# Optimization experiments

Hardware: AMD Instinct MI355X
Metric: run time of the kernel (lower is better)

## Reference

```python
import jax, jax.numpy as jnp
import numpy as np
import math

E_IN, E_OUT = 512, 96
B, QL, PL = 64, 128, 196

def _lin(k, shape):
    fan_in = shape[1]
    bound = 1.0 / math.sqrt(fan_in)
    k1, k2 = jax.random.split(k)
    W = jax.random.uniform(k1, shape, jnp.float32, -bound, bound)
    b = jax.random.uniform(k2, (shape[0],), jnp.float32, -bound, bound)
    return W, b

def setup_inputs() -> dict:
    key = jax.random.key(0)
    ks = jax.random.split(key, 16)
    inp = {
        'z_d_cls': jax.random.normal(ks[0], (B, E_IN), jnp.float32),
        'Z_d_tok': jax.random.normal(ks[1], (B, QL, E_IN), jnp.float32),
        'z_t_cls': jax.random.normal(ks[2], (B, E_IN), jnp.float32),
        'Z_t_tok': jax.random.normal(ks[3], (B, QL, E_IN), jnp.float32),
        'z_v_cls': jax.random.normal(ks[4], (B, E_IN), jnp.float32),
        'Z_v_patch': jax.random.normal(ks[5], (B, PL, E_IN), jnp.float32),
    }
    names = ['t_cls', 'd_cls', 'v_cls', 't_tok', 'v_patch', 'tgl_q', 'tgl_k', 'tgl_v']
    for i, n in enumerate(names):
        W, b = _lin(ks[6 + i], (E_OUT, E_IN))
        inp[f'W_{n}'] = W
        inp[f'b_{n}'] = b
    inp['ln_g'] = jnp.ones((E_OUT,), jnp.float32)
    inp['ln_b'] = jnp.zeros((E_OUT,), jnp.float32)
    return inp

def _l2n(x, eps=1e-6):
    return x / jnp.maximum(jnp.linalg.norm(x, axis=-1, keepdims=True), eps)

def _proj(x, W, b):
    return x @ W.T + b

def _layer_norm(x, g, b, eps=1e-5):
    mu = jnp.mean(x, axis=-1, keepdims=True)
    var = jnp.mean((x - mu) ** 2, axis=-1, keepdims=True)
    return (x - mu) / jnp.sqrt(var + eps) * g + b

def reference(z_d_cls, Z_d_tok, z_t_cls, Z_t_tok, z_v_cls, Z_v_patch,
              W_t_cls, b_t_cls, W_d_cls, b_d_cls, W_v_cls, b_v_cls,
              W_t_tok, b_t_tok, W_v_patch, b_v_patch,
              W_tgl_q, b_tgl_q, W_tgl_k, b_tgl_k, W_tgl_v, b_tgl_v,
              ln_g, ln_b):
    # --- TGG: global-global text/doc cosine sim [B, B]
    t = _l2n(_proj(z_t_cls, W_t_cls, b_t_cls))
    d = _l2n(_proj(z_d_cls, W_d_cls, b_d_cls))
    S_TGG = t @ d.T
    # --- TGL: cross-attention over all batch pairs
    Q = _proj(Z_d_tok, W_tgl_q, b_tgl_q)   # [b, q, h]
    K = _proj(Z_t_tok, W_tgl_k, b_tgl_k)   # [c, k, h]
    V = _proj(Z_t_tok, W_tgl_v, b_tgl_v)   # [c, k, h]
    scores = jnp.einsum('bqh,ckh->bcqk', Q, K) / math.sqrt(E_OUT)
    attn = jax.nn.softmax(scores, axis=-1)
    context = jnp.einsum('bcqk,ckh->bcqh', attn, V).mean(axis=2)  # [b, c, h]
    context = _layer_norm(context, ln_g, ln_b)
    S_TGL = jnp.einsum('ih,ijh->ij', d, _l2n(context))
    S_TIB = 0.5 * (S_TGG + S_TGL)
    # --- CGG: global-global text/vision cosine sim
    v = _l2n(_proj(z_v_cls, W_v_cls, b_v_cls))
    S_CGG = t @ v.T
    # --- CLL: token-patch max similarity
    t_tok = _l2n(_proj(Z_t_tok, W_t_tok, b_t_tok))        # [b, t, h]
    v_pat = _l2n(_proj(Z_v_patch, W_v_patch, b_v_patch))  # [c, p, h]
    sim = jnp.einsum('bth,cph->bctp', t_tok, v_pat)
    S_CLL = sim.max(axis=(-1, -2))
    S_CAB = 0.5 * (S_CGG + S_CLL)
    return S_TIB + S_CAB
```

## Files before the change

### kernel.cpp

```cpp
#include <hip/hip_runtime.h>
#include <hip/hip_bf16.h>
#include <math.h>

typedef __bf16 bf16;
typedef __attribute__((ext_vector_type(8))) __bf16 bf16x8;
typedef __attribute__((ext_vector_type(2))) float f32x2;
typedef __attribute__((ext_vector_type(4))) float f32x4;
typedef __attribute__((ext_vector_type(4))) unsigned int uint4v;

#define MFMA16(a, b, c) __builtin_amdgcn_mfma_f32_16x16x32_bf16(a, b, c, 0, 0, 0)

#define QSCALE 0.14724450f

__device__ __forceinline__ bf16x8 cvt8v(f32x4 lo, f32x4 hi) {
    bf16x8 r;
    r[0] = (bf16)lo[0]; r[1] = (bf16)lo[1]; r[2] = (bf16)lo[2]; r[3] = (bf16)lo[3];
    r[4] = (bf16)hi[0]; r[5] = (bf16)hi[1]; r[6] = (bf16)hi[2]; r[7] = (bf16)hi[3];
    return r;
}


struct ProjParams {
    const float* src[8];
    const float* W[8];
    const float* B[8];
    void* dst[8];
};

__global__ __launch_bounds__(256) void proj_kernel(ProjParams p) {
    int w = threadIdx.x >> 6, lane = threadIdx.x & 63;
    int gw = blockIdx.x * 4 + w;
    int m = lane & 15, quad = lane >> 4;

    int job, t0;
    if      (gw < 256)  { job = 3; t0 = gw; }
    else if (gw < 512)  { job = 4; t0 = gw - 256; }
    else if (gw < 768)  { job = 5; t0 = gw - 512; }
    else if (gw < 1024) { job = 6; t0 = gw - 768; }
    else if (gw < 1416) { job = 7; t0 = gw - 1024; }
    else if (gw < 1422) { int r = gw - 1416; job = r >> 1; t0 = r & 1; }
    else return;
    int r0 = t0 << 5;

    const float* X  = p.src[job] + (size_t)(r0 + m) * 512 + quad * 8;
    const float* Wf = p.W[job] + (size_t)m * 512 + quad * 8;

    f32x4 acc[2][6] = {};
    #pragma unroll
    for (int kk = 0; kk < 512; kk += 32) {
        bf16x8 a0 = cvt8v(*(const f32x4*)(X + kk),
                          *(const f32x4*)(X + kk + 4));
        bf16x8 a1 = cvt8v(*(const f32x4*)(X + 16 * 512 + kk),
                          *(const f32x4*)(X + 16 * 512 + kk + 4));
        #pragma unroll
        for (int nt = 0; nt < 6; nt++) {
            const float* wp = Wf + (size_t)nt * 16 * 512 + kk;
            bf16x8 b = cvt8v(*(const f32x4*)wp, *(const f32x4*)(wp + 4));
            acc[0][nt] = MFMA16(a0, b, acc[0][nt]);
            acc[1][nt] = MFMA16(a1, b, acc[1][nt]);
        }
    }

    bool  norm  = (job < 3) || (job >= 6);
    float scale = (job == 3) ? QSCALE : 1.0f;
    const float* Bv = p.B[job];
    float bb[6];
    #pragma unroll
    for (int nt = 0; nt < 6; nt++) bb[nt] = Bv[nt * 16 + m];

    #pragma unroll
    for (int rt = 0; rt < 2; rt++)
        #pragma unroll
        for (int nt = 0; nt < 6; nt++)
            #pragma unroll
            for (int r = 0; r < 4; r++)
                acc[rt][nt][r] = (acc[rt][nt][r] + bb[nt]) * scale;

    if (norm) {
        #pragma unroll
        for (int rt = 0; rt < 2; rt++)
            #pragma unroll
            for (int r = 0; r < 4; r++) {
                float s = 0.0f;
                #pragma unroll
                for (int nt = 0; nt < 6; nt++) s += acc[rt][nt][r] * acc[rt][nt][r];
                s += __shfl_xor(s, 1); s += __shfl_xor(s, 2);
                s += __shfl_xor(s, 4); s += __shfl_xor(s, 8);
                float inv = 1.0f / fmaxf(sqrtf(s), 1e-6f);
                #pragma unroll
                for (int nt = 0; nt < 6; nt++) acc[rt][nt][r] *= inv;
            }
    }

    if (job < 3) {
        float* dst = (float*)p.dst[job];
        #pragma unroll
        for (int rt = 0; rt < 2; rt++)
            #pragma unroll
            for (int r = 0; r < 4; r++)
                #pragma unroll
                for (int nt = 0; nt < 6; nt++)
                    dst[(size_t)(r0 + rt * 16 + quad * 4 + r) * 96 + nt * 16 + m] = acc[rt][nt][r];
    } else {
        bf16* dst = (bf16*)p.dst[job];
        #pragma unroll
        for (int rt = 0; rt < 2; rt++)
            #pragma unroll
            for (int r = 0; r < 4; r++)
                #pragma unroll
                for (int nt = 0; nt < 6; nt++)
                    dst[(size_t)(r0 + rt * 16 + quad * 4 + r) * 96 + nt * 16 + m] = (bf16)acc[rt][nt][r];
    }
}


__global__ __launch_bounds__(256) void attn_kernel(
    const bf16* __restrict__ Qg, const bf16* __restrict__ Kg, const bf16* __restrict__ Vg,
    float* __restrict__ Ctx)
{
    int pr = blockIdx.x;
    int b = pr >> 6, c = pr & 63;
    int tid = threadIdx.x, lane = tid & 63, w = tid >> 6;
    int m = lane & 15, quad = lane >> 4;
    const bf16* Q = Qg + (size_t)b * (128 * 96);
    const bf16* K = Kg + (size_t)c * (128 * 96);
    const bf16* V = Vg + (size_t)c * (128 * 96);

    __shared__ __align__(16) bf16 Klds[128 * 96];
    char* kb = (char*)Klds;
    #pragma unroll
    for (int it = 0; it < 6; it++) {
        int ch = it * 256 + tid;
        int row = ch / 12, seg = ch - row * 12;
        int addr = (row * 192 + seg * 16) ^ ((row & 7) << 4);
        *(uint4v*)(kb + addr) = *(const uint4v*)(K + ch * 8);
    }
    __syncthreads();

    int kx = (m & 7) << 4;
    f32x4 acc[2][8] = {};
    #pragma unroll
    for (int kk = 0; kk < 96; kk += 32) {
        bf16x8 a0 = *(const bf16x8*)(Q + (size_t)(w * 32 + m) * 96 + kk + quad * 8);
        bf16x8 a1 = *(const bf16x8*)(Q + (size_t)(w * 32 + 16 + m) * 96 + kk + quad * 8);
        #pragma unroll
        for (int nt = 0; nt < 8; nt++) {
            int addr = ((nt * 16 + m) * 192 + kk * 2 + quad * 16) ^ kx;
            bf16x8 bb = *(const bf16x8*)(kb + addr);
            acc[0][nt] = MFMA16(a0, bb, acc[0][nt]);
            acc[1][nt] = MFMA16(a1, bb, acc[1][nt]);
        }
    }

    unsigned vr[32];
    if (lane < 48) {
        #pragma unroll
        for (int r = 0; r < 32; r++)
            vr[r] = *(const unsigned*)(V + (size_t)(w * 32 + r) * 96 + lane * 2);
    }

    float wpart[8];
    #pragma unroll
    for (int nt = 0; nt < 8; nt++) wpart[nt] = 0.0f;
    #pragma unroll
    for (int mt = 0; mt < 2; mt++) {
        #pragma unroll
        for (int r = 0; r < 4; r++) {
            float tv[8]; float s = 0.0f;
            #pragma unroll
            for (int nt = 0; nt < 8; nt++) { tv[nt] = exp2f(acc[mt][nt][r]); s += tv[nt]; }
            s += __shfl_xor(s, 1); s += __shfl_xor(s, 2);
            s += __shfl_xor(s, 4); s += __shfl_xor(s, 8);
            float inv = __builtin_amdgcn_rcpf(s);
            #pragma unroll
            for (int nt = 0; nt < 8; nt++) wpart[nt] += tv[nt] * inv;
        }
    }
    #pragma unroll
    for (int nt = 0; nt < 8; nt++) {
        wpart[nt] += __shfl_xor(wpart[nt], 16);
        wpart[nt] += __shfl_xor(wpart[nt], 32);
    }
    __shared__ float wsum4[4][128];
    __shared__ float wk[128];
    __shared__ float ctxp[4][96];
    if (lane < 16) {
        #pragma unroll
        for (int nt = 0; nt < 8; nt++) wsum4[w][nt * 16 + lane] = wpart[nt];
    }
    __syncthreads();
    if (tid < 128) wk[tid] = wsum4[0][tid] + wsum4[1][tid] + wsum4[2][tid] + wsum4[3][tid];
    __syncthreads();
    {
        float c0 = 0.0f, c1 = 0.0f;
        if (lane < 48) {
            #pragma unroll
            for (int r = 0; r < 32; r++) {
                unsigned u = vr[r];
                float wkk = wk[w * 32 + r];
                c0 += wkk * __uint_as_float(u << 16);
                c1 += wkk * __uint_as_float(u & 0xffff0000u);
            }
            ctxp[w][lane * 2]     = c0;
            ctxp[w][lane * 2 + 1] = c1;
        }
    }
    __syncthreads();
    if (tid < 96)
        Ctx[(size_t)pr * 96 + tid] =
            (ctxp[0][tid] + ctxp[1][tid] + ctxp[2][tid] + ctxp[3][tid]) * (1.0f / 128.0f);
}


__global__ __launch_bounds__(256) void cll_kernel(
    const bf16* __restrict__ Tt, const bf16* __restrict__ Vp,
    const float* __restrict__ Ctx, const float* __restrict__ t,
    const float* __restrict__ d, const float* __restrict__ v,
    const float* __restrict__ ln_g, const float* __restrict__ ln_b,
    float* __restrict__ out)
{
    int c = blockIdx.x >> 3, bg = blockIdx.x & 7;
    int tid = threadIdx.x, lane = tid & 63, w = tid >> 6;
    int m = lane & 15, quad = lane >> 4;
    const bf16* P = Vp + (size_t)c * (196 * 96);

    __shared__ __align__(16) bf16 Plds[196 * 96];
    __shared__ float red[8][4];
    char* pb = (char*)Plds;
    for (int ch = tid; ch < 2352; ch += 256) {
        int row = ch / 12, seg = ch - row * 12;
        int addr = (row * 192 + seg * 16) ^ ((row & 7) << 4);
        *(uint4v*)(pb + addr) = *(const uint4v*)(P + ch * 8);
    }
    int rofs[13], rx[13];
    #pragma unroll
    for (int nt = 0; nt < 13; nt++) {
        int r = nt * 16 + m; if (r > 195) r = 195;
        rofs[nt] = r * 192 + quad * 16;
        rx[nt]   = (r & 7) << 4;
    }
    __syncthreads();

    for (int bi = 0; bi < 8; bi++) {
        const bf16* T = Tt + (size_t)(bg * 8 + bi) * (128 * 96);
        f32x4 acc[2][13] = {};
        #pragma unroll
        for (int kk = 0; kk < 96; kk += 32) {
            bf16x8 a0 = *(const bf16x8*)(T + (size_t)(w * 32 + m) * 96 + kk + quad * 8);
            bf16x8 a1 = *(const bf16x8*)(T + (size_t)(w * 32 + 16 + m) * 96 + kk + quad * 8);
            #pragma unroll
            for (int nt = 0; nt < 13; nt++) {
                bf16x8 bb = *(const bf16x8*)(pb + ((rofs[nt] + kk * 2) ^ rx[nt]));
                acc[0][nt] = MFMA16(a0, bb, acc[0][nt]);
                acc[1][nt] = MFMA16(a1, bb, acc[1][nt]);
            }
        }
        float mx = -3.4e38f;
        #pragma unroll
        for (int mt = 0; mt < 2; mt++)
            #pragma unroll
            for (int nt = 0; nt < 13; nt++)
                #pragma unroll
                for (int r = 0; r < 4; r++) mx = fmaxf(mx, acc[mt][nt][r]);
        #pragma unroll
        for (int dd = 1; dd < 64; dd <<= 1) mx = fmaxf(mx, __shfl_xor(mx, dd));
        if (lane == 0) red[bi][w] = mx;
    }
    __syncthreads();

    #pragma unroll
    for (int half = 0; half < 2; half++) {
        int bi = w + half * 4;
        int i  = bg * 8 + bi;
        int pr = i * 64 + c;
        float scll = fmaxf(fmaxf(red[bi][0], red[bi][1]), fmaxf(red[bi][2], red[bi][3]));
        bool act = lane < 48;
        float c0 = 0, c1 = 0, t0 = 0, t1 = 0;
        float dj0 = 0, dj1 = 0, di0 = 0, di1 = 0, v0 = 0, v1 = 0, g0 = 0, g1 = 0, bb0 = 0, bb1 = 0;
        if (act) {
            f32x2 cc  = *(const f32x2*)(Ctx + (size_t)pr * 96 + lane * 2);
            f32x2 tt  = *(const f32x2*)(t + i * 96 + lane * 2);
            f32x2 ddj = *(const f32x2*)(d + c * 96 + lane * 2);
            f32x2 ddi = *(const f32x2*)(d + i * 96 + lane * 2);
            f32x2 vv  = *(const f32x2*)(v + c * 96 + lane * 2);
            f32x2 gg  = *(const f32x2*)(ln_g + lane * 2);
            f32x2 bbv = *(const f32x2*)(ln_b + lane * 2);
            c0 = cc[0]; c1 = cc[1]; t0 = tt[0]; t1 = tt[1];
            dj0 = ddj[0]; dj1 = ddj[1]; di0 = ddi[0]; di1 = ddi[1];
            v0 = vv[0]; v1 = vv[1];
            g0 = gg[0]; g1 = gg[1]; bb0 = bbv[0]; bb1 = bbv[1];
        }
        float s = c0 + c1;
        #pragma unroll
        for (int k = 1; k < 64; k <<= 1) s += __shfl_xor(s, k);
        float mean = s * (1.0f / 96.0f);
        float e0 = act ? (c0 - mean) : 0.0f;
        float e1 = act ? (c1 - mean) : 0.0f;
        float q = e0 * e0 + e1 * e1;
        #pragma unroll
        for (int k = 1; k < 64; k <<= 1) q += __shfl_xor(q, k);
        float rstd = rsqrtf(q * (1.0f / 96.0f) + 1e-5f);
        float y0 = act ? (e0 * rstd * g0 + bb0) : 0.0f;
        float y1 = act ? (e1 * rstd * g1 + bb1) : 0.0f;
        float dot = y0 * di0 + y1 * di1;
        float ssq = y0 * y0 + y1 * y1;
        float tg  = t0 * dj0 + t1 * dj1;
        float cg  = t0 * v0 + t1 * v1;
        #pragma unroll
        for (int k = 1; k < 64; k <<= 1) {
            dot += __shfl_xor(dot, k); ssq += __shfl_xor(ssq, k);
            tg  += __shfl_xor(tg, k);  cg  += __shfl_xor(cg, k);
        }
        if (lane == 0) {
            float stgl = dot / fmaxf(sqrtf(ssq), 1e-6f);
            out[pr] = 0.5f * (tg + stgl) + 0.5f * (cg + scll);
        }
    }
}


extern "C" void kernel_launch(void* const* d_in, const int* in_sizes, int n_in,
                              void* d_out, int out_size, void* d_ws, size_t ws_size,
                              hipStream_t stream)
{
    (void)in_sizes; (void)n_in; (void)out_size; (void)ws_size;
    char* ws = (char*)d_ws;
    float* t     = (float*)(ws + 0);
    float* d     = (float*)(ws + 24576);
    float* v     = (float*)(ws + 49152);
    bf16* Qb = (bf16*)(ws + 892928);
    bf16* Kb = (bf16*)(ws + 892928 + 1572864);
    bf16* Vb = (bf16*)(ws + 892928 + 2 * 1572864);
    bf16* Tt = (bf16*)(ws + 892928 + 3 * 1572864);
    bf16* Vp = (bf16*)(ws + 892928 + 4 * 1572864);
    float* Ctx = (float*)(ws + 892928 + 4 * 1572864 + 2408448);

    ProjParams pp;
    pp.src[0] = (const float*)d_in[2];  pp.W[0] = (const float*)d_in[6];  pp.B[0] = (const float*)d_in[7];  pp.dst[0] = t;
    pp.src[1] = (const float*)d_in[0];  pp.W[1] = (const float*)d_in[8];  pp.B[1] = (const float*)d_in[9];  pp.dst[1] = d;
    pp.src[2] = (const float*)d_in[4];  pp.W[2] = (const float*)d_in[10]; pp.B[2] = (const float*)d_in[11]; pp.dst[2] = v;
    pp.src[3] = (const float*)d_in[1];  pp.W[3] = (const float*)d_in[16]; pp.B[3] = (const float*)d_in[17]; pp.dst[3] = Qb;
    pp.src[4] = (const float*)d_in[3];  pp.W[4] = (const float*)d_in[18]; pp.B[4] = (const float*)d_in[19]; pp.dst[4] = Kb;
    pp.src[5] = (const float*)d_in[3];  pp.W[5] = (const float*)d_in[20]; pp.B[5] = (const float*)d_in[21]; pp.dst[5] = Vb;
    pp.src[6] = (const float*)d_in[3];  pp.W[6] = (const float*)d_in[12]; pp.B[6] = (const float*)d_in[13]; pp.dst[6] = Tt;
    pp.src[7] = (const float*)d_in[5];  pp.W[7] = (const float*)d_in[14]; pp.B[7] = (const float*)d_in[15]; pp.dst[7] = Vp;
    hipLaunchKernelGGL(proj_kernel, dim3(356), dim3(256), 0, stream, pp);

    hipLaunchKernelGGL(attn_kernel, dim3(4096), dim3(256), 0, stream,
                       (const bf16*)Qb, (const bf16*)Kb, (const bf16*)Vb, Ctx);
    hipLaunchKernelGGL(cll_kernel, dim3(512), dim3(256), 0, stream,
                       (const bf16*)Tt, (const bf16*)Vp,
                       (const float*)Ctx, (const float*)t, (const float*)d, (const float*)v,
                       (const float*)d_in[22], (const float*)d_in[23], (float*)d_out);
}
```

Measured before the change: 264.5 us.

## Fuse projection, attention and CLL stages into one persistent kernel with grid barriers

Replaces the three kernel launches with one 256-block persistent kernel that separates its stages with atomic grid-wide barriers. It first converts the weights to bf16 once so the projection tiles read bf16 weights, then loops blocks over the projection, attention and CLL tiles. In attention each block keeps its K/V slice resident and reuses it over 16 query batches, using a padded LDS layout in place of the XOR swizzle. This removes launch gaps and repeated K/V loads, at the cost of a fixed 256-block grid that may underfill 256 CUs with 2 blocks per CU allowed, extra memset and barrier overhead, and deadlock risk if not all blocks are co-resident.

```diff
diff --git a/kernel.cpp b/kernel.cpp
--- a/kernel.cpp
+++ b/kernel.cpp
@@ -19,301 +19,314 @@
     return r;
 }
 
-
-struct ProjParams {
+__device__ __forceinline__ void grid_barrier(unsigned* bar, int slot, unsigned nblk, int tid) {
+    __syncthreads();
+    if (tid == 0) {
+        __threadfence();
+        __hip_atomic_fetch_add(&bar[slot], 1u, __ATOMIC_ACQ_REL, __HIP_MEMORY_SCOPE_AGENT);
+        while (__hip_atomic_load(&bar[slot], __ATOMIC_ACQUIRE, __HIP_MEMORY_SCOPE_AGENT) < nblk)
+            __builtin_amdgcn_s_sleep(2);
+        __threadfence();
+    }
+    __syncthreads();
+}
+
+struct MegaParams {
+    const float* W[8];
     const float* src[8];
-    const float* W[8];
     const float* B[8];
     void* dst[8];
+    bf16* Wb;
+    const bf16 *Qb, *Kb, *Vb, *Tt, *Vp;
+    float* Ctx;
+    const float *t, *d, *v, *ln_g, *ln_b;
+    float* out;
+    unsigned* bar;
 };
 
-__global__ __launch_bounds__(256) void proj_kernel(ProjParams p) {
-    int w = threadIdx.x >> 6, lane = threadIdx.x & 63;
-    int gw = blockIdx.x * 4 + w;
+
+__global__ __launch_bounds__(256, 2) void mega_kernel(MegaParams P) {
+    int tid = threadIdx.x, bid = blockIdx.x;
+    int w = tid >> 6, lane = tid & 63;
     int m = lane & 15, quad = lane >> 4;
-
-    int job, t0;
-    if      (gw < 256)  { job = 3; t0 = gw; }
-    else if (gw < 512)  { job = 4; t0 = gw - 256; }
-    else if (gw < 768)  { job = 5; t0 = gw - 512; }
-    else if (gw < 1024) { job = 6; t0 = gw - 768; }
-    else if (gw < 1416) { job = 7; t0 = gw - 1024; }
-    else if (gw < 1422) { int r = gw - 1416; job = r >> 1; t0 = r & 1; }
-    else return;
-    int r0 = t0 << 5;
-
-    const float* X  = p.src[job] + (size_t)(r0 + m) * 512 + quad * 8;
-    const float* Wf = p.W[job] + (size_t)m * 512 + quad * 8;
-
-    f32x4 acc[2][6] = {};
-    #pragma unroll
-    for (int kk = 0; kk < 512; kk += 32) {
-        bf16x8 a0 = cvt8v(*(const f32x4*)(X + kk),
-                          *(const f32x4*)(X + kk + 4));
-        bf16x8 a1 = cvt8v(*(const f32x4*)(X + 16 * 512 + kk),
-                          *(const f32x4*)(X + 16 * 512 + kk + 4));
-        #pragma unroll
-        for (int nt = 0; nt < 6; nt++) {
-            const float* wp = Wf + (size_t)nt * 16 * 512 + kk;
-            bf16x8 b = cvt8v(*(const f32x4*)wp, *(const f32x4*)(wp + 4));
-            acc[0][nt] = MFMA16(a0, b, acc[0][nt]);
-            acc[1][nt] = MFMA16(a1, b, acc[1][nt]);
-        }
-    }
-
-    bool  norm  = (job < 3) || (job >= 6);
-    float scale = (job == 3) ? QSCALE : 1.0f;
-    const float* Bv = p.B[job];
-    float bb[6];
-    #pragma unroll
-    for (int nt = 0; nt < 6; nt++) bb[nt] = Bv[nt * 16 + m];
-
-    #pragma unroll
-    for (int rt = 0; rt < 2; rt++)
-        #pragma unroll
-        for (int nt = 0; nt < 6; nt++)
-            #pragma unroll
-            for (int r = 0; r < 4; r++)
-                acc[rt][nt][r] = (acc[rt][nt][r] + bb[nt]) * scale;
-
-    if (norm) {
+    unsigned nblk = gridDim.x;
+
+    __shared__ __align__(16) char smem[37888];
+    bf16*  Klds  = (bf16*)smem;
+    float* wsum4 = (float*)(smem + 26624);
+    float* wk    = (float*)(smem + 28672);
+    float* ctxp  = (float*)(smem + 29184);
+    char*  pb    = smem;
+    float* red   = (float*)(smem + 37632);
+
+    {
+        int base = bid * 384;
+        for (int k = tid; k < 384; k += 256) {
+            int e4  = base + k;
+            int j   = e4 / 12288;
+            int off = (e4 - j * 12288) * 4;
+            f32x4 val = *(const f32x4*)(P.W[j] + off);
+            bf16* dst = P.Wb + j * 49152 + off;
+            dst[0] = (bf16)val[0]; dst[1] = (bf16)val[1];
+            dst[2] = (bf16)val[2]; dst[3] = (bf16)val[3];
+        }
+    }
+    grid_barrier(P.bar, 0, nblk, tid);
+
+    for (int tile = bid * 4 + w; tile < 1422; tile += 1024) {
+        int job, t0;
+        if      (tile < 256)  { job = 3; t0 = tile; }
+        else if (tile < 512)  { job = 4; t0 = tile - 256; }
+        else if (tile < 768)  { job = 5; t0 = tile - 512; }
+        else if (tile < 1024) { job = 6; t0 = tile - 768; }
+        else if (tile < 1416) { job = 7; t0 = tile - 1024; }
+        else                  { int r = tile - 1416; job = r >> 1; t0 = r & 1; }
+        int r0 = t0 << 5;
+        const float* X = P.src[job] + (size_t)(r0 + m) * 512 + quad * 8;
+        const bf16*  W = P.Wb + job * 49152 + (size_t)m * 512 + quad * 8;
+
+        f32x4 acc[2][6] = {};
+        #pragma unroll
+        for (int kk = 0; kk < 512; kk += 32) {
+            bf16x8 a0 = cvt8v(*(const f32x4*)(X + kk),
+                              *(const f32x4*)(X + kk + 4));
+            bf16x8 a1 = cvt8v(*(const f32x4*)(X + 16 * 512 + kk),
+                              *(const f32x4*)(X + 16 * 512 + kk + 4));
+            #pragma unroll
+            for (int nt = 0; nt < 6; nt++) {
+                bf16x8 b = *(const bf16x8*)(W + (size_t)nt * 16 * 512 + kk);
+                acc[0][nt] = MFMA16(a0, b, acc[0][nt]);
+                acc[1][nt] = MFMA16(a1, b, acc[1][nt]);
+            }
+        }
+        bool  norm  = (job < 3) || (job >= 6);
+        float scale = (job == 3) ? QSCALE : 1.0f;
+        const float* Bv = P.B[job];
+        float bb[6];
+        #pragma unroll
+        for (int nt = 0; nt < 6; nt++) bb[nt] = Bv[nt * 16 + m];
         #pragma unroll
         for (int rt = 0; rt < 2; rt++)
             #pragma unroll
-            for (int r = 0; r < 4; r++) {
-                float s = 0.0f;
-                #pragma unroll
-                for (int nt = 0; nt < 6; nt++) s += acc[rt][nt][r] * acc[rt][nt][r];
-                s += __shfl_xor(s, 1); s += __shfl_xor(s, 2);
-                s += __shfl_xor(s, 4); s += __shfl_xor(s, 8);
-                float inv = 1.0f / fmaxf(sqrtf(s), 1e-6f);
-                #pragma unroll
-                for (int nt = 0; nt < 6; nt++) acc[rt][nt][r] *= inv;
-            }
-    }
-
-    if (job < 3) {
-        float* dst = (float*)p.dst[job];
-        #pragma unroll
-        for (int rt = 0; rt < 2; rt++)
-            #pragma unroll
-            for (int r = 0; r < 4; r++)
-                #pragma unroll
-                for (int nt = 0; nt < 6; nt++)
-                    dst[(size_t)(r0 + rt * 16 + quad * 4 + r) * 96 + nt * 16 + m] = acc[rt][nt][r];
-    } else {
-        bf16* dst = (bf16*)p.dst[job];
-        #pragma unroll
-        for (int rt = 0; rt < 2; rt++)
-            #pragma unroll
-            for (int r = 0; r < 4; r++)
-                #pragma unroll
-                for (int nt = 0; nt < 6; nt++)
-                    dst[(size_t)(r0 + rt * 16 + quad * 4 + r) * 96 + nt * 16 + m] = (bf16)acc[rt][nt][r];
-    }
-}
-
-
-__global__ __launch_bounds__(256) void attn_kernel(
-    const bf16* __restrict__ Qg, const bf16* __restrict__ Kg, const bf16* __restrict__ Vg,
-    float* __restrict__ Ctx)
-{
-    int pr = blockIdx.x;
-    int b = pr >> 6, c = pr & 63;
-    int tid = threadIdx.x, lane = tid & 63, w = tid >> 6;
-    int m = lane & 15, quad = lane >> 4;
-    const bf16* Q = Qg + (size_t)b * (128 * 96);
-    const bf16* K = Kg + (size_t)c * (128 * 96);
-    const bf16* V = Vg + (size_t)c * (128 * 96);
-
-    __shared__ __align__(16) bf16 Klds[128 * 96];
-    char* kb = (char*)Klds;
-    #pragma unroll
-    for (int it = 0; it < 6; it++) {
-        int ch = it * 256 + tid;
-        int row = ch / 12, seg = ch - row * 12;
-        int addr = (row * 192 + seg * 16) ^ ((row & 7) << 4);
-        *(uint4v*)(kb + addr) = *(const uint4v*)(K + ch * 8);
-    }
-    __syncthreads();
-
-    int kx = (m & 7) << 4;
-    f32x4 acc[2][8] = {};
-    #pragma unroll
-    for (int kk = 0; kk < 96; kk += 32) {
-        bf16x8 a0 = *(const bf16x8*)(Q + (size_t)(w * 32 + m) * 96 + kk + quad * 8);
-        bf16x8 a1 = *(const bf16x8*)(Q + (size_t)(w * 32 + 16 + m) * 96 + kk + quad * 8);
-        #pragma unroll
-        for (int nt = 0; nt < 8; nt++) {
-            int addr = ((nt * 16 + m) * 192 + kk * 2 + quad * 16) ^ kx;
-            bf16x8 bb = *(const bf16x8*)(kb + addr);
-            acc[0][nt] = MFMA16(a0, bb, acc[0][nt]);
-            acc[1][nt] = MFMA16(a1, bb, acc[1][nt]);
-        }
-    }
-
-    unsigned vr[32];
-    if (lane < 48) {
-        #pragma unroll
-        for (int r = 0; r < 32; r++)
-            vr[r] = *(const unsigned*)(V + (size_t)(w * 32 + r) * 96 + lane * 2);
-    }
-
-    float wpart[8];
-    #pragma unroll
-    for (int nt = 0; nt < 8; nt++) wpart[nt] = 0.0f;
-    #pragma unroll
-    for (int mt = 0; mt < 2; mt++) {
-        #pragma unroll
-        for (int r = 0; r < 4; r++) {
-            float tv[8]; float s = 0.0f;
-            #pragma unroll
-            for (int nt = 0; nt < 8; nt++) { tv[nt] = exp2f(acc[mt][nt][r]); s += tv[nt]; }
-            s += __shfl_xor(s, 1); s += __shfl_xor(s, 2);
-            s += __shfl_xor(s, 4); s += __shfl_xor(s, 8);
-            float inv = __builtin_amdgcn_rcpf(s);
-            #pragma unroll
-            for (int nt = 0; nt < 8; nt++) wpart[nt] += tv[nt] * inv;
-        }
-    }
-    #pragma unroll
-    for (int nt = 0; nt < 8; nt++) {
-        wpart[nt] += __shfl_xor(wpart[nt], 16);
-        wpart[nt] += __shfl_xor(wpart[nt], 32);
-    }
-    __shared__ float wsum4[4][128];
-    __shared__ float wk[128];
-    __shared__ float ctxp[4][96];
-    if (lane < 16) {
-        #pragma unroll
-        for (int nt = 0; nt < 8; nt++) wsum4[w][nt * 16 + lane] = wpart[nt];
-    }
-    __syncthreads();
-    if (tid < 128) wk[tid] = wsum4[0][tid] + wsum4[1][tid] + wsum4[2][tid] + wsum4[3][tid];
-    __syncthreads();
+            for (int nt = 0; nt < 6; nt++)
+                #pragma unroll
+                for (int r = 0; r < 4; r++)
+                    acc[rt][nt][r] = (acc[rt][nt][r] + bb[nt]) * scale;
+        if (norm) {
+            #pragma unroll
+            for (int rt = 0; rt < 2; rt++)
+                #pragma unroll
+                for (int r = 0; r < 4; r++) {
+                    float s = 0.0f;
+                    #pragma unroll
+                    for (int nt = 0; nt < 6; nt++) s += acc[rt][nt][r] * acc[rt][nt][r];
+                    s += __shfl_xor(s, 1); s += __shfl_xor(s, 2);
+                    s += __shfl_xor(s, 4); s += __shfl_xor(s, 8);
+                    float inv = 1.0f / fmaxf(sqrtf(s), 1e-6f);
+                    #pragma unroll
+                    for (int nt = 0; nt < 6; nt++) acc[rt][nt][r] *= inv;
+                }
+        }
+        if (job < 3) {
+            float* dst = (float*)P.dst[job];
+            #pragma unroll
+            for (int rt = 0; rt < 2; rt++)
+                #pragma unroll
+                for (int r = 0; r < 4; r++)
+                    #pragma unroll
+                    for (int nt = 0; nt < 6; nt++)
+                        dst[(size_t)(r0 + rt * 16 + quad * 4 + r) * 96 + nt * 16 + m] = acc[rt][nt][r];
+        } else {
+            bf16* dst = (bf16*)P.dst[job];
+            #pragma unroll
+            for (int rt = 0; rt < 2; rt++)
+                #pragma unroll
+                for (int r = 0; r < 4; r++)
+                    #pragma unroll
+                    for (int nt = 0; nt < 6; nt++)
+                        dst[(size_t)(r0 + rt * 16 + quad * 4 + r) * 96 + nt * 16 + m] = (bf16)acc[rt][nt][r];
+        }
+    }
+    grid_barrier(P.bar, 1, nblk, tid);
+
     {
-        float c0 = 0.0f, c1 = 0.0f;
+        int c = bid & 63;
+        const bf16* K = P.Kb + (size_t)c * (128 * 96);
+        const bf16* V = P.Vb + (size_t)c * (128 * 96);
+        #pragma unroll
+        for (int it = 0; it < 6; it++) {
+            int ch = it * 256 + tid;
+            int row = ch / 12, seg = ch - row * 12;
+            *(uint4v*)(Klds + row * 104 + seg * 8) = *(const uint4v*)(K + ch * 8);
+        }
+        unsigned vr[32];
         if (lane < 48) {
             #pragma unroll
-            for (int r = 0; r < 32; r++) {
-                unsigned u = vr[r];
-                float wkk = wk[w * 32 + r];
-                c0 += wkk * __uint_as_float(u << 16);
-                c1 += wkk * __uint_as_float(u & 0xffff0000u);
-            }
-            ctxp[w][lane * 2]     = c0;
-            ctxp[w][lane * 2 + 1] = c1;
-        }
-    }
-    __syncthreads();
-    if (tid < 96)
-        Ctx[(size_t)pr * 96 + tid] =
-            (ctxp[0][tid] + ctxp[1][tid] + ctxp[2][tid] + ctxp[3][tid]) * (1.0f / 128.0f);
-}
-
-
-__global__ __launch_bounds__(256) void cll_kernel(
-    const bf16* __restrict__ Tt, const bf16* __restrict__ Vp,
-    const float* __restrict__ Ctx, const float* __restrict__ t,
-    const float* __restrict__ d, const float* __restrict__ v,
-    const float* __restrict__ ln_g, const float* __restrict__ ln_b,
-    float* __restrict__ out)
-{
-    int c = blockIdx.x >> 3, bg = blockIdx.x & 7;
-    int tid = threadIdx.x, lane = tid & 63, w = tid >> 6;
-    int m = lane & 15, quad = lane >> 4;
-    const bf16* P = Vp + (size_t)c * (196 * 96);
-
-    __shared__ __align__(16) bf16 Plds[196 * 96];
-    __shared__ float red[8][4];
-    char* pb = (char*)Plds;
-    for (int ch = tid; ch < 2352; ch += 256) {
-        int row = ch / 12, seg = ch - row * 12;
-        int addr = (row * 192 + seg * 16) ^ ((row & 7) << 4);
-        *(uint4v*)(pb + addr) = *(const uint4v*)(P + ch * 8);
-    }
-    int rofs[13], rx[13];
-    #pragma unroll
-    for (int nt = 0; nt < 13; nt++) {
-        int r = nt * 16 + m; if (r > 195) r = 195;
-        rofs[nt] = r * 192 + quad * 16;
-        rx[nt]   = (r & 7) << 4;
-    }
-    __syncthreads();
-
-    for (int bi = 0; bi < 8; bi++) {
-        const bf16* T = Tt + (size_t)(bg * 8 + bi) * (128 * 96);
-        f32x4 acc[2][13] = {};
-        #pragma unroll
-        for (int kk = 0; kk < 96; kk += 32) {
-            bf16x8 a0 = *(const bf16x8*)(T + (size_t)(w * 32 + m) * 96 + kk + quad * 8);
-            bf16x8 a1 = *(const bf16x8*)(T + (size_t)(w * 32 + 16 + m) * 96 + kk + quad * 8);
-            #pragma unroll
-            for (int nt = 0; nt < 13; nt++) {
-                bf16x8 bb = *(const bf16x8*)(pb + ((rofs[nt] + kk * 2) ^ rx[nt]));
-                acc[0][nt] = MFMA16(a0, bb, acc[0][nt]);
-                acc[1][nt] = MFMA16(a1, bb, acc[1][nt]);
-            }
-        }
-        float mx = -3.4e38f;
-        #pragma unroll
-        for (int mt = 0; mt < 2; mt++)
-            #pragma unroll
-            for (int nt = 0; nt < 13; nt++)
-                #pragma unroll
-                for (int r = 0; r < 4; r++) mx = fmaxf(mx, acc[mt][nt][r]);
-        #pragma unroll
-        for (int dd = 1; dd < 64; dd <<= 1) mx = fmaxf(mx, __shfl_xor(mx, dd));
-        if (lane == 0) red[bi][w] = mx;
-    }
-    __syncthreads();
-
-    #pragma unroll
-    for (int half = 0; half < 2; half++) {
-        int bi = w + half * 4;
-        int i  = bg * 8 + bi;
-        int pr = i * 64 + c;
-        float scll = fmaxf(fmaxf(red[bi][0], red[bi][1]), fmaxf(red[bi][2], red[bi][3]));
-        bool act = lane < 48;
-        float c0 = 0, c1 = 0, t0 = 0, t1 = 0;
-        float dj0 = 0, dj1 = 0, di0 = 0, di1 = 0, v0 = 0, v1 = 0, g0 = 0, g1 = 0, bb0 = 0, bb1 = 0;
-        if (act) {
-            f32x2 cc  = *(const f32x2*)(Ctx + (size_t)pr * 96 + lane * 2);
-            f32x2 tt  = *(const f32x2*)(t + i * 96 + lane * 2);
-            f32x2 ddj = *(const f32x2*)(d + c * 96 + lane * 2);
-            f32x2 ddi = *(const f32x2*)(d + i * 96 + lane * 2);
-            f32x2 vv  = *(const f32x2*)(v + c * 96 + lane * 2);
-            f32x2 gg  = *(const f32x2*)(ln_g + lane * 2);
-            f32x2 bbv = *(const f32x2*)(ln_b + lane * 2);
-            c0 = cc[0]; c1 = cc[1]; t0 = tt[0]; t1 = tt[1];
-            dj0 = ddj[0]; dj1 = ddj[1]; di0 = ddi[0]; di1 = ddi[1];
-            v0 = vv[0]; v1 = vv[1];
-            g0 = gg[0]; g1 = gg[1]; bb0 = bbv[0]; bb1 = bbv[1];
-        }
-        float s = c0 + c1;
-        #pragma unroll
-        for (int k = 1; k < 64; k <<= 1) s += __shfl_xor(s, k);
-        float mean = s * (1.0f / 96.0f);
-        float e0 = act ? (c0 - mean) : 0.0f;
-        float e1 = act ? (c1 - mean) : 0.0f;
-        float q = e0 * e0 + e1 * e1;
-        #pragma unroll
-        for (int k = 1; k < 64; k <<= 1) q += __shfl_xor(q, k);
-        float rstd = rsqrtf(q * (1.0f / 96.0f) + 1e-5f);
-        float y0 = act ? (e0 * rstd * g0 + bb0) : 0.0f;
-        float y1 = act ? (e1 * rstd * g1 + bb1) : 0.0f;
-        float dot = y0 * di0 + y1 * di1;
-        float ssq = y0 * y0 + y1 * y1;
-        float tg  = t0 * dj0 + t1 * dj1;
-        float cg  = t0 * v0 + t1 * v1;
-        #pragma unroll
-        for (int k = 1; k < 64; k <<= 1) {
-            dot += __shfl_xor(dot, k); ssq += __shfl_xor(ssq, k);
-            tg  += __shfl_xor(tg, k);  cg  += __shfl_xor(cg, k);
-        }
-        if (lane == 0) {
-            float stgl = dot / fmaxf(sqrtf(ssq), 1e-6f);
-            out[pr] = 0.5f * (tg + stgl) + 0.5f * (cg + scll);
+            for (int r = 0; r < 32; r++)
+                vr[r] = *(const unsigned*)(V + (size_t)(w * 32 + r) * 96 + lane * 2);
+        }
+        __syncthreads();
+
+        for (int i = 0; i < 16; i++) {
+            int b = (bid >> 6) + 4 * i;
+            int pr = b * 64 + c;
+            const bf16* Q = P.Qb + (size_t)b * (128 * 96);
+
+            f32x4 acc[2][8] = {};
+            #pragma unroll
+            for (int kk = 0; kk < 96; kk += 32) {
+                bf16x8 a0 = *(const bf16x8*)(Q + (size_t)(w * 32 + m) * 96 + kk + quad * 8);
+                bf16x8 a1 = *(const bf16x8*)(Q + (size_t)(w * 32 + 16 + m) * 96 + kk + quad * 8);
+                #pragma unroll
+                for (int nt = 0; nt < 8; nt++) {
+                    bf16x8 bbk = *(const bf16x8*)(Klds + (nt * 16 + m) * 104 + kk + quad * 8);
+                    acc[0][nt] = MFMA16(a0, bbk, acc[0][nt]);
+                    acc[1][nt] = MFMA16(a1, bbk, acc[1][nt]);
+                }
+            }
+            float wpart[8];
+            #pragma unroll
+            for (int nt = 0; nt < 8; nt++) wpart[nt] = 0.0f;
+            #pragma unroll
+            for (int mt = 0; mt < 2; mt++) {
+                #pragma unroll
+                for (int r = 0; r < 4; r++) {
+                    float tv[8]; float s = 0.0f;
+                    #pragma unroll
+                    for (int nt = 0; nt < 8; nt++) { tv[nt] = exp2f(acc[mt][nt][r]); s += tv[nt]; }
+                    s += __shfl_xor(s, 1); s += __shfl_xor(s, 2);
+                    s += __shfl_xor(s, 4); s += __shfl_xor(s, 8);
+                    float inv = 1.0f / s;
+                    #pragma unroll
+                    for (int nt = 0; nt < 8; nt++) wpart[nt] += tv[nt] * inv;
+                }
+            }
+            #pragma unroll
+            for (int nt = 0; nt < 8; nt++) {
+                wpart[nt] += __shfl_xor(wpart[nt], 16);
+                wpart[nt] += __shfl_xor(wpart[nt], 32);
+            }
+            if (lane < 16) {
+                #pragma unroll
+                for (int nt = 0; nt < 8; nt++) wsum4[w * 128 + nt * 16 + lane] = wpart[nt];
+            }
+            __syncthreads();
+            if (tid < 128)
+                wk[tid] = wsum4[tid] + wsum4[128 + tid] + wsum4[256 + tid] + wsum4[384 + tid];
+            __syncthreads();
+            if (lane < 48) {
+                float c0 = 0.0f, c1 = 0.0f;
+                #pragma unroll
+                for (int r = 0; r < 32; r++) {
+                    unsigned u = vr[r];
+                    float wkk = wk[w * 32 + r];
+                    c0 += wkk * __uint_as_float(u << 16);
+                    c1 += wkk * __uint_as_float(u & 0xffff0000u);
+                }
+                ctxp[w * 96 + lane * 2]     = c0;
+                ctxp[w * 96 + lane * 2 + 1] = c1;
+            }
+            __syncthreads();
+            if (tid < 96)
+                P.Ctx[(size_t)pr * 96 + tid] =
+                    (ctxp[tid] + ctxp[96 + tid] + ctxp[192 + tid] + ctxp[288 + tid]) * (1.0f / 128.0f);
+            __syncthreads();
+        }
+    }
+    grid_barrier(P.bar, 2, nblk, tid);
+
+    {
+        int c = bid >> 2, bg2 = bid & 3;
+        const bf16* Pv = P.Vp + (size_t)c * (196 * 96);
+        for (int ch = tid; ch < 2352; ch += 256) {
+            int row = ch / 12, seg = ch - row * 12;
+            int addr = (row * 192 + seg * 16) ^ ((row & 7) << 4);
+            *(uint4v*)(pb + addr) = *(const uint4v*)(Pv + ch * 8);
+        }
+        int rofs[13], rx[13];
+        #pragma unroll
+        for (int nt = 0; nt < 13; nt++) {
+            int r = nt * 16 + m; if (r > 195) r = 195;
+            rofs[nt] = r * 192 + quad * 16;
+            rx[nt]   = (r & 7) << 4;
+        }
+        __syncthreads();
+
+        for (int bi = 0; bi < 16; bi++) {
+            const bf16* T = P.Tt + (size_t)(bg2 * 16 + bi) * (128 * 96);
+            f32x4 acc[2][13] = {};
+            #pragma unroll
+            for (int kk = 0; kk < 96; kk += 32) {
+                bf16x8 a0 = *(const bf16x8*)(T + (size_t)(w * 32 + m) * 96 + kk + quad * 8);
+                bf16x8 a1 = *(const bf16x8*)(T + (size_t)(w * 32 + 16 + m) * 96 + kk + quad * 8);
+                #pragma unroll
+                for (int nt = 0; nt < 13; nt++) {
+                    bf16x8 bbp = *(const bf16x8*)(pb + ((rofs[nt] + kk * 2) ^ rx[nt]));
+                    acc[0][nt] = MFMA16(a0, bbp, acc[0][nt]);
+                    acc[1][nt] = MFMA16(a1, bbp, acc[1][nt]);
+                }
+            }
+            float mx = -3.4e38f;
+            #pragma unroll
+            for (int mt = 0; mt < 2; mt++)
+                #pragma unroll
+                for (int nt = 0; nt < 13; nt++)
+                    #pragma unroll
+                    for (int r = 0; r < 4; r++) mx = fmaxf(mx, acc[mt][nt][r]);
+            #pragma unroll
+            for (int dd = 1; dd < 64; dd <<= 1) mx = fmaxf(mx, __shfl_xor(mx, dd));
+            if (lane == 0) red[bi * 4 + w] = mx;
+        }
+        __syncthreads();
+
+        #pragma unroll
+        for (int half = 0; half < 4; half++) {
+            int bi = w + half * 4;
+            int i  = bg2 * 16 + bi;
+            int pr = i * 64 + c;
+            float scll = fmaxf(fmaxf(red[bi * 4 + 0], red[bi * 4 + 1]),
+                               fmaxf(red[bi * 4 + 2], red[bi * 4 + 3]));
+            bool act = lane < 48;
+            float c0 = 0, c1 = 0, t0 = 0, t1 = 0;
+            float dj0 = 0, dj1 = 0, di0 = 0, di1 = 0, v0 = 0, v1 = 0, g0 = 0, g1 = 0, bb0 = 0, bb1 = 0;
+            if (act) {
+                f32x2 cc  = *(const f32x2*)(P.Ctx + (size_t)pr * 96 + lane * 2);
+                f32x2 tt  = *(const f32x2*)(P.t + i * 96 + lane * 2);
+                f32x2 ddj = *(const f32x2*)(P.d + c * 96 + lane * 2);
+                f32x2 ddi = *(const f32x2*)(P.d + i * 96 + lane * 2);
+                f32x2 vv  = *(const f32x2*)(P.v + c * 96 + lane * 2);
+                f32x2 gg  = *(const f32x2*)(P.ln_g + lane * 2);
+                f32x2 bbv = *(const f32x2*)(P.ln_b + lane * 2);
+                c0 = cc[0]; c1 = cc[1]; t0 = tt[0]; t1 = tt[1];
+                dj0 = ddj[0]; dj1 = ddj[1]; di0 = ddi[0]; di1 = ddi[1];
+                v0 = vv[0]; v1 = vv[1];
+                g0 = gg[0]; g1 = gg[1]; bb0 = bbv[0]; bb1 = bbv[1];
+            }
+            float s = c0 + c1;
+            #pragma unroll
+            for (int k = 1; k < 64; k <<= 1) s += __shfl_xor(s, k);
+            float mean = s * (1.0f / 96.0f);
+            float e0 = act ? (c0 - mean) : 0.0f;
+            float e1 = act ? (c1 - mean) : 0.0f;
+            float q = e0 * e0 + e1 * e1;
+            #pragma unroll
+            for (int k = 1; k < 64; k <<= 1) q += __shfl_xor(q, k);
+            float rstd = rsqrtf(q * (1.0f / 96.0f) + 1e-5f);
+            float y0 = act ? (e0 * rstd * g0 + bb0) : 0.0f;
+            float y1 = act ? (e1 * rstd * g1 + bb1) : 0.0f;
+            float dot = y0 * di0 + y1 * di1;
+            float ssq = y0 * y0 + y1 * y1;
+            float tg  = t0 * dj0 + t1 * dj1;
+            float cg  = t0 * v0 + t1 * v1;
+            #pragma unroll
+            for (int k = 1; k < 64; k <<= 1) {
+                dot += __shfl_xor(dot, k); ssq += __shfl_xor(ssq, k);
+                tg  += __shfl_xor(tg, k);  cg  += __shfl_xor(cg, k);
+            }
+            if (lane == 0) {
+                float stgl = dot / fmaxf(sqrtf(ssq), 1e-6f);
+                P.out[pr] = 0.5f * (tg + stgl) + 0.5f * (cg + scll);
+            }
         }
     }
 }
@@ -325,9 +338,11 @@
 {
     (void)in_sizes; (void)n_in; (void)out_size; (void)ws_size;
     char* ws = (char*)d_ws;
-    float* t     = (float*)(ws + 0);
-    float* d     = (float*)(ws + 24576);
-    float* v     = (float*)(ws + 49152);
+    float* t   = (float*)(ws + 0);
+    float* d   = (float*)(ws + 24576);
+    float* v   = (float*)(ws + 49152);
+    unsigned* bar = (unsigned*)(ws + 73728);
+    bf16* Wb = (bf16*)(ws + 106496);
     bf16* Qb = (bf16*)(ws + 892928);
     bf16* Kb = (bf16*)(ws + 892928 + 1572864);
     bf16* Vb = (bf16*)(ws + 892928 + 2 * 1572864);
@@ -335,21 +350,32 @@
     bf16* Vp = (bf16*)(ws + 892928 + 4 * 1572864);
     float* Ctx = (float*)(ws + 892928 + 4 * 1572864 + 2408448);
 
-    ProjParams pp;
-    pp.src[0] = (const float*)d_in[2];  pp.W[0] = (const float*)d_in[6];  pp.B[0] = (const float*)d_in[7];  pp.dst[0] = t;
-    pp.src[1] = (const float*)d_in[0];  pp.W[1] = (const float*)d_in[8];  pp.B[1] = (const float*)d_in[9];  pp.dst[1] = d;
-    pp.src[2] = (const float*)d_in[4];  pp.W[2] = (const float*)d_in[10]; pp.B[2] = (const float*)d_in[11]; pp.dst[2] = v;
-    pp.src[3] = (const float*)d_in[1];  pp.W[3] = (const float*)d_in[16]; pp.B[3] = (const float*)d_in[17]; pp.dst[3] = Qb;
-    pp.src[4] = (const float*)d_in[3];  pp.W[4] = (const float*)d_in[18]; pp.B[4] = (const float*)d_in[19]; pp.dst[4] = Kb;
-    pp.src[5] = (const float*)d_in[3];  pp.W[5] = (const float*)d_in[20]; pp.B[5] = (const float*)d_in[21]; pp.dst[5] = Vb;
-    pp.src[6] = (const float*)d_in[3];  pp.W[6] = (const float*)d_in[12]; pp.B[6] = (const float*)d_in[13]; pp.dst[6] = Tt;
-    pp.src[7] = (const float*)d_in[5];  pp.W[7] = (const float*)d_in[14]; pp.B[7] = (const float*)d_in[15]; pp.dst[7] = Vp;
-    hipLaunchKernelGGL(proj_kernel, dim3(356), dim3(256), 0, stream, pp);
-
-    hipLaunchKernelGGL(attn_kernel, dim3(4096), dim3(256), 0, stream,
-                       (const bf16*)Qb, (const bf16*)Kb, (const bf16*)Vb, Ctx);
-    hipLaunchKernelGGL(cll_kernel, dim3(512), dim3(256), 0, stream,
-                       (const bf16*)Tt, (const bf16*)Vp,
-                       (const float*)Ctx, (const float*)t, (const float*)d, (const float*)v,
-                       (const float*)d_in[22], (const float*)d_in[23], (float*)d_out);
+    MegaParams P;
+    P.W[0] = (const float*)d_in[6];
+    P.W[1] = (const float*)d_in[8];
+    P.W[2] = (const float*)d_in[10];
+    P.W[3] = (const float*)d_in[16];
+    P.W[4] = (const float*)d_in[18];
+    P.W[5] = (const float*)d_in[20];
+    P.W[6] = (const float*)d_in[12];
+    P.W[7] = (const float*)d_in[14];
+    P.src[0] = (const float*)d_in[2];  P.B[0] = (const float*)d_in[7];  P.dst[0] = t;
+    P.src[1] = (const float*)d_in[0];  P.B[1] = (const float*)d_in[9];  P.dst[1] = d;
+    P.src[2] = (const float*)d_in[4];  P.B[2] = (const float*)d_in[11]; P.dst[2] = v;
+    P.src[3] = (const float*)d_in[1];  P.B[3] = (const float*)d_in[17]; P.dst[3] = Qb;
+    P.src[4] = (const float*)d_in[3];  P.B[4] = (const float*)d_in[19]; P.dst[4] = Kb;
+    P.src[5] = (const float*)d_in[3];  P.B[5] = (const float*)d_in[21]; P.dst[5] = Vb;
+    P.src[6] = (const float*)d_in[3];  P.B[6] = (const float*)d_in[13]; P.dst[6] = Tt;
+    P.src[7] = (const float*)d_in[5];  P.B[7] = (const float*)d_in[15]; P.dst[7] = Vp;
+    P.Wb = Wb;
+    P.Qb = Qb; P.Kb = Kb; P.Vb = Vb; P.Tt = Tt; P.Vp = Vp;
+    P.Ctx = Ctx;
+    P.t = t; P.d = d; P.v = v;
+    P.ln_g = (const float*)d_in[22];
+    P.ln_b = (const float*)d_in[23];
+    P.out = (float*)d_out;
+    P.bar = bar;
+
+    hipMemsetAsync(bar, 0, 16, stream);
+    hipLaunchKernelGGL(mega_kernel, dim3(256), dim3(256), 0, stream, P);
 }
```

Measured after the change: 372.0 us. +40.6%, slower.
